# Kernel tuning notes

Hardware: AMD Instinct MI355X
Metric: run time of the kernel (lower is better)

## Reference

```python
import jax, jax.numpy as jnp
import numpy as np

B, W, G, E, NI, K = 2048, 8192, 8, 128, 16, 15


def setup_inputs() -> dict:
    key = jax.random.key(0)
    ks = jax.random.split(key, 12)
    wavelengths_nm = jnp.linspace(300.0, 400.0, W, dtype=jnp.float32)
    # Rayleigh optical depth (Hansen & Travis style approximation), AMF=1 column
    lam_um = wavelengths_nm / 1000.0
    rayleigh_od = (0.008569 * lam_um ** -4
                   * (1.0 + 0.0113 * lam_um ** -2 + 0.00013 * lam_um ** -4)).astype(jnp.float32)
    return {
        "gas_columns": jax.random.uniform(ks[0], (B, G), jnp.float32),
        "instrument_ids": jax.random.randint(ks[1], (B,), 0, NI),
        "nuisance_latent": jax.random.normal(ks[2], (B, G), jnp.float32),
        "air_mass": 1.0 + 2.0 * jax.random.uniform(ks[3], (B,), jnp.float32),
        "wavelengths_nm": wavelengths_nm,
        "absorption": 0.1 * jax.random.uniform(ks[4], (G, W), jnp.float32),
        "continuum_basis": 0.05 * jax.random.normal(ks[5], (G + 1, W), jnp.float32),
        "rayleigh_od": rayleigh_od,
        "embed_table": jax.random.normal(ks[6], (NI, E), jnp.float32),
        "w1": jax.random.normal(ks[7], (E + G, 64), jnp.float32) / np.sqrt(E + G),
        "b1": jnp.zeros((64,), jnp.float32),
        "w2": jax.random.normal(ks[8], (64, 7), jnp.float32) / 8.0,
        "b2": jnp.zeros((7,), jnp.float32),
    }


def _gaussian_kernel(width_px, kernel_size):
    half = (kernel_size - 1) / 2
    pos = jnp.linspace(-half, half, kernel_size, dtype=width_px.dtype)  # [K]
    k = jnp.exp(-0.5 * (pos[None, :] / (width_px[:, None] + 1e-6)) ** 2)  # [B,K]
    return k / k.sum(axis=1, keepdims=True)


def _forward(gas_columns, nuisance_latent, air_mass, wavelengths_nm, absorption,
             continuum_basis, rayleigh_od, embed_table, w1, b1, w2, b2,
             instrument_ids):
    b = gas_columns.shape[0]
    am = air_mass[:, None]                                   # [B,1]
    scaled = gas_columns * am                                # [B,G]
    optical_depth = scaled @ absorption                      # [B,W]
    ones = jnp.ones((b, 1), gas_columns.dtype)
    continuum = jnp.concatenate([gas_columns, ones], axis=1) @ continuum_basis  # [B,W]
    differential = optical_depth + continuum + am * rayleigh_od[None, :]

    # nuisance MLP on [latent, embedding]
    embed = embed_table[instrument_ids]                      # [B,E]
    nin = jnp.concatenate([nuisance_latent, embed], axis=-1)
    h = jax.nn.gelu(nin @ w1 + b1, approximate=False)
    p = h @ w2 + b2                                          # [B,7]

    gain = jax.nn.softplus(p[:, 0]) + 0.001
    offset = p[:, 1]
    woff = 0.05 * jnp.tanh(p[:, 2])
    wscale = 1.0 + 0.005 * jnp.tanh(p[:, 3])
    lsf = jnp.clip(jax.nn.softplus(p[:, 4]) + 0.001, 0.2, 5.0)
    stray = jax.nn.sigmoid(p[:, 5]) * 0.05
    nonlin = 0.02 * jnp.tanh(p[:, 6])

    # per-sample wavelength shift/scale + linear resampling
    new_wl = wavelengths_nm[None, :] * wscale[:, None] + woff[:, None]  # [B,W]
    differential = jax.vmap(lambda wq, d: jnp.interp(wq, wavelengths_nm, d))(new_wl, differential)

    # per-sample Gaussian LSF convolution (replicate padding)
    kernel = _gaussian_kernel(lsf, K)                        # [B,K]
    pad = K // 2
    padded = jnp.pad(differential, ((0, 0), (pad, pad)), mode='edge')  # [B,W+K-1]
    n = differential.shape[1]
    convolved = sum(padded[:, k:k + n] * kernel[:, k:k + 1] for k in range(K))

    counts = jnp.exp(-convolved)
    post = gain[:, None] * counts + offset[:, None]
    total_nl = jnp.clip(nonlin, -0.04, 0.04)                 # instrument nonlinearity = 0
    nl_counts = post + total_nl[:, None] * post ** 2
    total_stray = jnp.clip(stray, 0.0, 0.2)                  # instrument stray = 0
    simulated = (1.0 - total_stray[:, None]) * nl_counts \
        + total_stray[:, None] * nl_counts.mean(axis=1, keepdims=True)
    return simulated


def reference(gas_columns, instrument_ids, nuisance_latent, air_mass,
              wavelengths_nm, absorption, continuum_basis, rayleigh_od,
              embed_table, w1, b1, w2, b2):
    return _forward(gas_columns, nuisance_latent, air_mass, wavelengths_nm,
                    absorption, continuum_basis, rayleigh_od, embed_table,
                    w1, b1, w2, b2, instrument_ids)
```

## Files before the change

kernel.cpp:

```cpp
#include <hip/hip_runtime.h>

#define W_ 8192
#define NBATCH 2048
#define NT 256
#define NWAVE 4
#define SEGW 2048
#define CCH 256
#define NCHW 8
#define IRW 272

typedef unsigned short u16_t;
typedef _Float16 h2v __attribute__((ext_vector_type(2)));

__device__ __forceinline__ u16_t f2h(float x){ _Float16 h=(_Float16)x; return __builtin_bit_cast(u16_t,h); }
__device__ __forceinline__ float h2f(u16_t u){ return (float)__builtin_bit_cast(_Float16,u); }
__device__ __forceinline__ unsigned pk2(float a,float b){ return (unsigned)f2h(a)|((unsigned)f2h(b)<<16); }
__device__ __forceinline__ float dot2u(unsigned a,unsigned b,float c){
#if __has_builtin(__builtin_amdgcn_fdot2)
  return __builtin_amdgcn_fdot2(__builtin_bit_cast(h2v,a),__builtin_bit_cast(h2v,b),c,false);
#else
  h2v ha=__builtin_bit_cast(h2v,a), hb=__builtin_bit_cast(h2v,b);
  return c+(float)ha[0]*(float)hb[0]+(float)ha[1]*(float)hb[1];
#endif
}
__device__ __forceinline__ unsigned pkrtz(float a,float b){
#if __has_builtin(__builtin_amdgcn_cvt_pkrtz)
  return __builtin_bit_cast(unsigned, __builtin_amdgcn_cvt_pkrtz(a,b));
#else
  return pk2(a,b);
#endif
}
__device__ __forceinline__ unsigned alignb(unsigned hi, unsigned lo){
#if __has_builtin(__builtin_amdgcn_alignbit)
  return __builtin_amdgcn_alignbit(hi, lo, 16);
#else
  return (lo >> 16) | (hi << 16);
#endif
}
__device__ __forceinline__ float softplusf(float x){ return fmaxf(x,0.f)+log1pf(expf(-fabsf(x))); }
__device__ __forceinline__ unsigned rflv(unsigned v){
  return (unsigned)__builtin_amdgcn_readfirstlane((int)v);
}
__device__ __forceinline__ float rflvf(float v){
  return __builtin_bit_cast(float, __builtin_amdgcn_readfirstlane(__builtin_bit_cast(int, v)));
}

__global__ __launch_bounds__(256, 2)
void doas_prep(const float* __restrict__ absn, const float* __restrict__ cbn,
               const float* __restrict__ ray, const int* __restrict__ iid,
               const float* __restrict__ nuis, const float* __restrict__ emb,
               const float* __restrict__ w1, const float* __restrict__ b1,
               const float* __restrict__ w2, const float* __restrict__ b2,
               unsigned* __restrict__ Tp, float* __restrict__ params){
  const int tid = threadIdx.x;
  const int b = blockIdx.x;
  __shared__ float hS[4][64];
  __shared__ float pS[4][8];

  if (b < 32){
    const int w = b*256 + tid;
    #pragma unroll
    for (int q=0;q<4;++q) Tp[q*W_+w]     = pk2(absn[(2*q)*W_+w], absn[(2*q+1)*W_+w]);
    #pragma unroll
    for (int q=0;q<4;++q) Tp[(4+q)*W_+w] = pk2(cbn[(2*q)*W_+w],  cbn[(2*q+1)*W_+w]);
    Tp[8*W_+w] = pk2(cbn[8*W_+w], ray[w]);
  }

  {
    const int rl = tid >> 6, j = tid & 63;
    const int r = b*4 + rl;
    const int id = iid[r];
    float acc = b1[j];
    const float* nrow = nuis + (size_t)r * 8;
    #pragma unroll
    for (int i = 0; i < 8; ++i) acc = fmaf(nrow[i], w1[i*64 + j], acc);
    const float* erow = emb + (size_t)id * 128;
    for (int i = 0; i < 128; ++i) acc = fmaf(erow[i], w1[(8+i)*64 + j], acc);
    hS[rl][j] = 0.5f * acc * (1.0f + erff(acc * 0.70710678118654752f));
  }
  __syncthreads();
  if (tid < 4*7){
    const int rl = tid / 7, k = tid % 7;
    float p = b2[k];
    for (int j = 0; j < 64; ++j) p = fmaf(hS[rl][j], w2[j*7+k], p);
    pS[rl][k] = p;
  }
  __syncthreads();
  if (tid < 4){
    const int rl = tid;
    const int r = b*4 + rl;
    float p0=pS[rl][0], p1=pS[rl][1], p2=pS[rl][2], p3=pS[rl][3],
          p4=pS[rl][4], p5=pS[rl][5], p6=pS[rl][6];
    float gainv = softplusf(p0) + 0.001f;
    float offv  = p1;
    float woffv = 0.05f * tanhf(p2);
    float wscv  = 1.0f + 0.005f * tanhf(p3);
    float lsf   = fminf(fmaxf(softplusf(p4) + 0.001f, 0.2f), 5.0f);
    float strv  = fminf(fmaxf((1.0f/(1.0f+expf(-p5))) * 0.05f, 0.0f), 0.2f);
    float nlin  = fminf(fmaxf(0.02f * tanhf(p6), -0.04f), 0.04f);
    float iw = 1.0f/(lsf + 1e-6f);
    float ks[15]; float ksum = 0.f;
    #pragma unroll
    for (int k2=0;k2<15;++k2){ float pp=(float)(k2-7)*iw; float e=expf(-0.5f*pp*pp); ks[k2]=e; ksum+=e; }
    float inv = 1.0f/ksum;
    float* pr = params + (size_t)r*16;
    unsigned* pu = (unsigned*)pr;
    #pragma unroll
    for (int i=0;i<7;++i) pu[i] = pk2(ks[2*i]*inv, ks[2*i+1]*inv);
    pu[7] = pk2(ks[14]*inv, 0.0f);
    pr[9]  = wscv;
    pr[10] = (300.0f*(wscv - 1.0f) + woffv) * (8191.0f/100.0f);
    pr[11] = gainv; pr[12] = offv; pr[13] = nlin; pr[14] = strv;
    pr[15] = 0.f;
  }
}

template<bool CLO, bool CHI>
__device__ __forceinline__ void interp_chunk(int cbase, int l, const unsigned* __restrict__ rU,
                                             unsigned* __restrict__ irowU,
                                             float wscale, float posoff){
  #pragma unroll
  for (int it=0; it<3; ++it){
    const int pi = it*64 + l;
    if (pi < 136){
      float v2[2];
      #pragma unroll
      for (int u=0;u<2;++u){
        int j = cbase + 2*pi + u;
        if (CLO) j = max(j, 0);
        if (CHI) j = min(j, W_-1);
        float pos = fmaf((float)j, wscale, posoff);
        if (CLO) pos = fmaxf(pos, 0.0f);
        if (CHI) pos = fminf(pos, 8191.0f);
        int i0 = (int)pos;
        if (CHI) i0 = min(i0, W_-2);
        const float fr = pos - (float)i0;
        const int m = i0 >> 1;
        const unsigned u0 = rU[m];
        const unsigned u1 = rU[m+1];
        const unsigned hu0 = u0 >> 16;
        const bool odd = (i0 & 1);
        const unsigned ua = odd ? hu0 : u0;
        const unsigned ub = odd ? u1  : hu0;
        const float d0 = h2f((u16_t)ua);
        const float d1 = h2f((u16_t)ub);
        v2[u] = fmaf(fr, d1-d0, d0);
      }
      irowU[pi] = pkrtz(v2[0], v2[1]);
    }
  }
}

__global__ __launch_bounds__(NT, 2)
void doas_main7(const unsigned* __restrict__ Tp, const float* __restrict__ gas,
                const float* __restrict__ air, const float* __restrict__ params,
                float* __restrict__ out){
  __shared__ u16_t rowH[W_ + 16];
  __shared__ u16_t irowS[NWAVE][IRW];
  __shared__ float wsumS[NWAVE];

  const int tid = threadIdx.x;
  const int row = blockIdx.x;
  const int wid = tid >> 6, l = tid & 63;
  const int segbase = wid * SEGW;

  unsigned csg[9];
  {
    const float am = air[row];
    const float* gfp = gas + (size_t)row * 8;
    #pragma unroll
    for (int q=0;q<4;++q) csg[q]   = rflv(pk2(gfp[2*q]*am, gfp[2*q+1]*am));
    #pragma unroll
    for (int q=0;q<4;++q) csg[4+q] = rflv(pk2(gfp[2*q],    gfp[2*q+1]));
    csg[8] = rflv(pk2(1.0f, am));
  }

  const float* pr = params + (size_t)row * 16;
  const unsigned* pu = (const unsigned*)pr;
  unsigned kwp[7];
  #pragma unroll
  for (int i=0;i<7;++i) kwp[i] = rflv(pu[i]);
  const unsigned k14lo = rflv(pu[7]);
  const float wscale = rflvf(pr[9]),  posoff = rflvf(pr[10]);
  const float gainv  = rflvf(pr[11]), offv   = rflvf(pr[12]);
  const float nlin   = rflvf(pr[13]), strv   = rflvf(pr[14]);

  unsigned* rowHU = (unsigned*)rowH;
  #pragma unroll
  for (int it=0; it<8; ++it){
    const int e0 = it*1024 + tid*4;
    uint4 dq[9];
    #pragma unroll
    for (int q=0;q<9;++q) dq[q] = *(const uint4*)(Tp + q*W_ + e0);
    float a0=0.f, a1=0.f, a2=0.f, a3=0.f;
    #pragma unroll
    for (int q=0;q<9;++q){
      a0 = dot2u(dq[q].x, csg[q], a0);
      a1 = dot2u(dq[q].y, csg[q], a1);
      a2 = dot2u(dq[q].z, csg[q], a2);
      a3 = dot2u(dq[q].w, csg[q], a3);
    }
    *(uint2*)(rowHU + (e0 >> 1)) = make_uint2(pkrtz(a0,a1), pkrtz(a2,a3));
  }
  __syncthreads();

  const unsigned* rU = (const unsigned*)rowH;
  u16_t* irow = &irowS[wid][0];
  unsigned* irowU = (unsigned*)irow;

  float accsum = 0.f;
  unsigned nlp[NCHW][2];

  #pragma unroll
  for (int c = 0; c < NCHW; ++c) {
    const int cs = segbase + c*CCH;
    const int cbase = cs - 8;
    if (wid == 0 && c == 0)
      interp_chunk<true,false>(cbase, l, rU, irowU, wscale, posoff);
    else if (wid == NWAVE-1 && c == NCHW-1)
      interp_chunk<false,true>(cbase, l, rU, irowU, wscale, posoff);
    else
      interp_chunk<false,false>(cbase, l, rU, irowU, wscale, posoff);
    __builtin_amdgcn_wave_barrier();
    {
      const uint2* p2 = (const uint2*)irowU + l;
      const uint2 A = p2[0], B = p2[1], C = p2[2], D = p2[3], E = p2[4];
      unsigned q[10] = {A.x,A.y, B.x,B.y, C.x,C.y, D.x,D.y, E.x,E.y};
      unsigned sh[9];
      #pragma unroll
      for (int m=0;m<9;++m) sh[m] = alignb(q[m+1], q[m]);
      float nlv[4];
      #pragma unroll
      for (int t=0;t<4;++t){
        float cv = 0.f;
        if ((t & 1) == 0){
          const int b0 = t >> 1;
          #pragma unroll
          for (int i=0;i<7;++i) cv = dot2u(sh[b0+i], kwp[i], cv);
          cv = dot2u(sh[b0+7], k14lo, cv);
        } else {
          const int b0 = (t+1) >> 1;
          #pragma unroll
          for (int i=0;i<7;++i) cv = dot2u(q[b0+i], kwp[i], cv);
          cv = dot2u(q[b0+7], k14lo, cv);
        }
        const float counts = __expf(-cv);
        const float post = fmaf(gainv, counts, offv);
        const float v = fmaf(nlin*post, post, post);
        accsum += v;
        nlv[t] = v;
      }
      nlp[c][0] = pkrtz(nlv[0], nlv[1]);
      nlp[c][1] = pkrtz(nlv[2], nlv[3]);
    }
    __builtin_amdgcn_wave_barrier();
  }

  float s = accsum;
  #pragma unroll
  for (int off2 = 32; off2 >= 1; off2 >>= 1) s += __shfl_down(s, off2);
  if (l == 0) wsumS[wid] = s;
  __syncthreads();
  const float meanv = (wsumS[0]+wsumS[1]+wsumS[2]+wsumS[3]) * (1.0f/8192.0f);

  {
    const float aa = 1.0f - strv;
    const float bb = strv * meanv;
    float* orow = out + (size_t)row * W_;
    #pragma unroll
    for (int c = 0; c < NCHW; ++c) {
      const unsigned u0 = nlp[c][0], u1 = nlp[c][1];
      float4 o0;
      o0.x = fmaf(aa, h2f((u16_t)(u0 & 0xffffu)), bb);
      o0.y = fmaf(aa, h2f((u16_t)(u0 >> 16)),     bb);
      o0.z = fmaf(aa, h2f((u16_t)(u1 & 0xffffu)), bb);
      o0.w = fmaf(aa, h2f((u16_t)(u1 >> 16)),     bb);
      *(float4*)(orow + segbase + c*CCH + 4*l) = o0;
    }
  }
}

__global__ __launch_bounds__(256, 2)
void doas_mono(const float* __restrict__ gas, const int* __restrict__ iid,
               const float* __restrict__ nuis, const float* __restrict__ air,
               const float* __restrict__ absn, const float* __restrict__ cbn,
               const float* __restrict__ ray, const float* __restrict__ emb,
               const float* __restrict__ w1, const float* __restrict__ b1,
               const float* __restrict__ w2, const float* __restrict__ b2,
               float* __restrict__ out)
{
  __shared__ u16_t ringS[4][2048];
  __shared__ u16_t irowS2[4][544];
  __shared__ float hS[64];
  __shared__ float pS[8];
  __shared__ float scalS[52];
  __shared__ float wsumS[4];

  const int tid = threadIdx.x;
  const int row = blockIdx.x;

  if (tid < 64) {
    const int j = tid;
    const int id = iid[row];
    float acc = b1[j];
    const float* nrow = nuis + (size_t)row * 8;
    #pragma unroll
    for (int i = 0; i < 8; ++i) acc = fmaf(nrow[i], w1[i*64 + j], acc);
    const float* erow = emb + (size_t)id * 128;
    for (int i = 0; i < 128; ++i) acc = fmaf(erow[i], w1[(8+i)*64 + j], acc);
    hS[j] = 0.5f * acc * (1.0f + erff(acc * 0.70710678118654752f));
  }
  __syncthreads();
  if (tid < 7) {
    float p = b2[tid];
    for (int j = 0; j < 64; ++j) p = fmaf(hS[j], w2[j*7+tid], p);
    pS[tid] = p;
  }
  __syncthreads();
  if (tid == 0) {
    float p0=pS[0], p1=pS[1], p2=pS[2], p3=pS[3], p4=pS[4], p5=pS[5], p6=pS[6];
    float gainv = softplusf(p0) + 0.001f;
    float offv  = p1;
    float woffv = 0.05f * tanhf(p2);
    float wscv  = 1.0f + 0.005f * tanhf(p3);
    float lsf   = fminf(fmaxf(softplusf(p4) + 0.001f, 0.2f), 5.0f);
    float strv  = fminf(fmaxf((1.0f/(1.0f+expf(-p5))) * 0.05f, 0.0f), 0.2f);
    float nlin  = fminf(fmaxf(0.02f * tanhf(p6), -0.04f), 0.04f);
    float iw = 1.0f/(lsf + 1e-6f);
    float ks[15]; float ksum = 0.f;
    #pragma unroll
    for (int k2=0;k2<15;++k2){ float pp=(float)(k2-7)*iw; float e=expf(-0.5f*pp*pp); ks[k2]=e; ksum+=e; }
    float inv = 1.0f/ksum;
    scalS[15] = wscv;
    scalS[16] = (300.0f*(wscv - 1.0f) + woffv) * (8191.0f/100.0f);
    scalS[17] = gainv; scalS[18] = offv; scalS[19] = nlin; scalS[20] = strv;
    scalS[22] = air[row];
    unsigned* su = (unsigned*)scalS;
    #pragma unroll
    for (int i=0;i<7;++i) su[32+i] = pk2(ks[2*i]*inv, ks[2*i+1]*inv);
    su[39] = pk2(ks[14]*inv, 0.0f);
    su[40] = pk2(0.0f, ks[14]*inv);
    #pragma unroll
    for (int g=0; g<8; ++g) scalS[23+g] = gas[(size_t)row*8+g];
  }
  __syncthreads();

  const int wid = tid >> 6, l = tid & 63;
  const int segbase = wid * 2048;
  const unsigned* scalU = (const unsigned*)scalS;
  unsigned kwp[7];
  #pragma unroll
  for (int i=0;i<7;++i) kwp[i] = rflv(scalU[32+i]);
  const unsigned k14lo = rflv(scalU[39]), k14hi = rflv(scalU[40]);
  const float wscale = scalS[15], posoff = scalS[16];
  const float gainv  = scalS[17], offv   = scalS[18];
  const float nlin   = scalS[19], strv   = scalS[20];

  u16_t* ring = &ringS[wid][0];
  unsigned* ringU = (unsigned*)ring;
  u16_t* irow = &irowS2[wid][0];
  unsigned* irowU = (unsigned*)irow;

  auto do_diff = [&](int s){
    const int sbase = segbase - 256 + (s << 9);
    #pragma unroll
    for (int it=0; it<4; ++it){
      const int e0 = sbase + ((it*64 + l) << 1);
      const int eL = min(max(e0, 0), W_-2);
      const float am = scalS[22];
      float a0=0.f, a1=0.f;
      #pragma unroll
      for (int g=0; g<8; ++g){
        const float cg = scalS[23+g];
        const float ca = cg*am;
        a0 = fmaf(ca, absn[g*W_+eL],   a0); a0 = fmaf(cg, cbn[g*W_+eL],   a0);
        a1 = fmaf(ca, absn[g*W_+eL+1], a1); a1 = fmaf(cg, cbn[g*W_+eL+1], a1);
      }
      a0 += cbn[8*W_+eL]   + am*ray[eL];
      a1 += cbn[8*W_+eL+1] + am*ray[eL+1];
      ringU[((unsigned)e0 & 2047) >> 1] = pkrtz(a0, a1);
    }
  };

  float accsum = 0.f;
  unsigned nlp[4][4];

  do_diff(0); do_diff(1);
  __builtin_amdgcn_wave_barrier();

  #pragma unroll
  for (int c = 0; c < 4; ++c) {
    if (c < 3) do_diff(c+2);
    __builtin_amdgcn_wave_barrier();
    {
      const int cbase = segbase + (c << 9) - 8;
      #pragma unroll
      for (int it = 0; it < 5; ++it) {
        const int pi = it*64 + l;
        if (pi < 264) {
          float v2[2];
          #pragma unroll
          for (int u=0; u<2; ++u){
            const int j = cbase + 2*pi + u;
            const int jc = min(max(j, 0), W_-1);
            float pos = fmaf((float)jc, wscale, posoff);
            pos = fminf(fmaxf(pos, 0.0f), 8191.0f);
            const int i0 = min((int)pos, W_-2);
            const float fr = pos - (float)i0;
            const float d0 = h2f(ring[ i0    & 2047]);
            const float d1 = h2f(ring[(i0+1) & 2047]);
            v2[u] = fmaf(fr, d1-d0, d0);
          }
          irowU[pi] = pkrtz(v2[0], v2[1]);
        }
      }
    }
    __builtin_amdgcn_wave_barrier();
    {
      const uint4* qp = (const uint4*)irow + l;
      const uint4 A = qp[0], B = qp[1], C = qp[2];
      unsigned q[12] = {A.x,A.y,A.z,A.w, B.x,B.y,B.z,B.w, C.x,C.y,C.z,C.w};
      unsigned sh[10];
      #pragma unroll
      for (int m=0;m<10;++m) sh[m] = alignb(q[m+1], q[m]);
      float nlv[8];
      #pragma unroll
      for (int t=0;t<8;++t){
        const int s2 = t >> 1;
        float cv = 0.f;
        if ((t & 1) == 0){
          #pragma unroll
          for (int i=0;i<7;++i) cv = dot2u(sh[s2+i], kwp[i], cv);
          cv = dot2u(q[s2+7], k14hi, cv);
        } else {
          #pragma unroll
          for (int i=0;i<7;++i) cv = dot2u(q[s2+1+i], kwp[i], cv);
          cv = dot2u(q[s2+8], k14lo, cv);
        }
        const float counts = __expf(-cv);
        const float post = fmaf(gainv, counts, offv);
        const float v = fmaf(nlin*post, post, post);
        accsum += v;
        nlv[t] = v;
      }
      nlp[c][0] = pkrtz(nlv[0], nlv[1]);
      nlp[c][1] = pkrtz(nlv[2], nlv[3]);
      nlp[c][2] = pkrtz(nlv[4], nlv[5]);
      nlp[c][3] = pkrtz(nlv[6], nlv[7]);
    }
    __builtin_amdgcn_wave_barrier();
  }

  float s = accsum;
  #pragma unroll
  for (int off2 = 32; off2 >= 1; off2 >>= 1) s += __shfl_down(s, off2);
  if (l == 0) wsumS[wid] = s;
  __syncthreads();
  const float meanv = (wsumS[0]+wsumS[1]+wsumS[2]+wsumS[3]) * (1.0f/8192.0f);

  {
    const float aa = 1.0f - strv;
    const float bb = strv * meanv;
    float* orow = out + (size_t)row * W_;
    #pragma unroll
    for (int c = 0; c < 4; ++c) {
      const unsigned u0 = nlp[c][0], u1 = nlp[c][1], u2 = nlp[c][2], u3 = nlp[c][3];
      float4 o0, o1;
      o0.x = fmaf(aa, h2f((u16_t)(u0 & 0xffffu)), bb);
      o0.y = fmaf(aa, h2f((u16_t)(u0 >> 16)),     bb);
      o0.z = fmaf(aa, h2f((u16_t)(u1 & 0xffffu)), bb);
      o0.w = fmaf(aa, h2f((u16_t)(u1 >> 16)),     bb);
      o1.x = fmaf(aa, h2f((u16_t)(u2 & 0xffffu)), bb);
      o1.y = fmaf(aa, h2f((u16_t)(u2 >> 16)),     bb);
      o1.z = fmaf(aa, h2f((u16_t)(u3 & 0xffffu)), bb);
      o1.w = fmaf(aa, h2f((u16_t)(u3 >> 16)),     bb);
      float* dst = orow + segbase + (c << 9) + 8*l;
      *(float4*)(dst)     = o0;
      *(float4*)(dst + 4) = o1;
    }
  }
}

extern "C" void kernel_launch(void* const* d_in, const int* in_sizes, int n_in,
                              void* d_out, int out_size, void* d_ws, size_t ws_size,
                              hipStream_t stream) {
  const float* gas  = (const float*)d_in[0];
  const int*   iid  = (const int*)d_in[1];
  const float* nuis = (const float*)d_in[2];
  const float* air  = (const float*)d_in[3];
  const float* wl   = (const float*)d_in[4];
  const float* absn = (const float*)d_in[5];
  const float* cbn  = (const float*)d_in[6];
  const float* ray  = (const float*)d_in[7];
  const float* emb  = (const float*)d_in[8];
  const float* w1   = (const float*)d_in[9];
  const float* b1   = (const float*)d_in[10];
  const float* w2   = (const float*)d_in[11];
  const float* b2   = (const float*)d_in[12];
  float* out = (float*)d_out;
  (void)in_sizes; (void)n_in; (void)out_size; (void)wl;

  const size_t packBytes = (size_t)9 * W_ * 4;
  const size_t parBytes  = (size_t)NBATCH * 16 * 4;

  if (ws_size >= packBytes + parBytes) {
    unsigned* Tp  = (unsigned*)d_ws;
    float* params = (float*)((char*)d_ws + packBytes);
    hipLaunchKernelGGL(doas_prep, dim3(NBATCH/4), dim3(256), 0, stream,
                       absn, cbn, ray, iid, nuis, emb, w1, b1, w2, b2, Tp, params);
    hipLaunchKernelGGL(doas_main7, dim3(NBATCH), dim3(NT), 0, stream,
                       Tp, gas, air, params, out);
  } else {
    hipLaunchKernelGGL(doas_mono, dim3(NBATCH), dim3(256), 0, stream,
                       gas, iid, nuis, air, absn, cbn, ray, emb, w1, b1, w2, b2, out);
  }
}
```

Before: 51.62 us.

## Fuse nuisance MLP into main kernel and store differential row as fp32 in LDS

```diff
diff --git a/kernel.cpp b/kernel.cpp
--- a/kernel.cpp
+++ b/kernel.cpp
@@ -45,78 +45,19 @@
   return __builtin_bit_cast(float, __builtin_amdgcn_readfirstlane(__builtin_bit_cast(int, v)));
 }
 
-__global__ __launch_bounds__(256, 2)
-void doas_prep(const float* __restrict__ absn, const float* __restrict__ cbn,
-               const float* __restrict__ ray, const int* __restrict__ iid,
-               const float* __restrict__ nuis, const float* __restrict__ emb,
-               const float* __restrict__ w1, const float* __restrict__ b1,
-               const float* __restrict__ w2, const float* __restrict__ b2,
-               unsigned* __restrict__ Tp, float* __restrict__ params){
-  const int tid = threadIdx.x;
-  const int b = blockIdx.x;
-  __shared__ float hS[4][64];
-  __shared__ float pS[4][8];
-
-  if (b < 32){
-    const int w = b*256 + tid;
-    #pragma unroll
-    for (int q=0;q<4;++q) Tp[q*W_+w]     = pk2(absn[(2*q)*W_+w], absn[(2*q+1)*W_+w]);
-    #pragma unroll
-    for (int q=0;q<4;++q) Tp[(4+q)*W_+w] = pk2(cbn[(2*q)*W_+w],  cbn[(2*q+1)*W_+w]);
-    Tp[8*W_+w] = pk2(cbn[8*W_+w], ray[w]);
-  }
-
-  {
-    const int rl = tid >> 6, j = tid & 63;
-    const int r = b*4 + rl;
-    const int id = iid[r];
-    float acc = b1[j];
-    const float* nrow = nuis + (size_t)r * 8;
-    #pragma unroll
-    for (int i = 0; i < 8; ++i) acc = fmaf(nrow[i], w1[i*64 + j], acc);
-    const float* erow = emb + (size_t)id * 128;
-    for (int i = 0; i < 128; ++i) acc = fmaf(erow[i], w1[(8+i)*64 + j], acc);
-    hS[rl][j] = 0.5f * acc * (1.0f + erff(acc * 0.70710678118654752f));
-  }
-  __syncthreads();
-  if (tid < 4*7){
-    const int rl = tid / 7, k = tid % 7;
-    float p = b2[k];
-    for (int j = 0; j < 64; ++j) p = fmaf(hS[rl][j], w2[j*7+k], p);
-    pS[rl][k] = p;
-  }
-  __syncthreads();
-  if (tid < 4){
-    const int rl = tid;
-    const int r = b*4 + rl;
-    float p0=pS[rl][0], p1=pS[rl][1], p2=pS[rl][2], p3=pS[rl][3],
-          p4=pS[rl][4], p5=pS[rl][5], p6=pS[rl][6];
-    float gainv = softplusf(p0) + 0.001f;
-    float offv  = p1;
-    float woffv = 0.05f * tanhf(p2);
-    float wscv  = 1.0f + 0.005f * tanhf(p3);
-    float lsf   = fminf(fmaxf(softplusf(p4) + 0.001f, 0.2f), 5.0f);
-    float strv  = fminf(fmaxf((1.0f/(1.0f+expf(-p5))) * 0.05f, 0.0f), 0.2f);
-    float nlin  = fminf(fmaxf(0.02f * tanhf(p6), -0.04f), 0.04f);
-    float iw = 1.0f/(lsf + 1e-6f);
-    float ks[15]; float ksum = 0.f;
-    #pragma unroll
-    for (int k2=0;k2<15;++k2){ float pp=(float)(k2-7)*iw; float e=expf(-0.5f*pp*pp); ks[k2]=e; ksum+=e; }
-    float inv = 1.0f/ksum;
-    float* pr = params + (size_t)r*16;
-    unsigned* pu = (unsigned*)pr;
-    #pragma unroll
-    for (int i=0;i<7;++i) pu[i] = pk2(ks[2*i]*inv, ks[2*i+1]*inv);
-    pu[7] = pk2(ks[14]*inv, 0.0f);
-    pr[9]  = wscv;
-    pr[10] = (300.0f*(wscv - 1.0f) + woffv) * (8191.0f/100.0f);
-    pr[11] = gainv; pr[12] = offv; pr[13] = nlin; pr[14] = strv;
-    pr[15] = 0.f;
-  }
+__global__ __launch_bounds__(64, 4)
+void doas_pack(const float* __restrict__ absn, const float* __restrict__ cbn,
+               const float* __restrict__ ray, unsigned* __restrict__ Tp){
+  const int w = blockIdx.x*64 + threadIdx.x;
+  #pragma unroll
+  for (int q=0;q<4;++q) Tp[q*W_+w]     = pk2(absn[(2*q)*W_+w], absn[(2*q+1)*W_+w]);
+  #pragma unroll
+  for (int q=0;q<4;++q) Tp[(4+q)*W_+w] = pk2(cbn[(2*q)*W_+w],  cbn[(2*q+1)*W_+w]);
+  Tp[8*W_+w] = pk2(cbn[8*W_+w], ray[w]);
 }
 
 template<bool CLO, bool CHI>
-__device__ __forceinline__ void interp_chunk(int cbase, int l, const unsigned* __restrict__ rU,
+__device__ __forceinline__ void interp_chunk(int cbase, int l, const float* __restrict__ rF,
                                              unsigned* __restrict__ irowU,
                                              float wscale, float posoff){
   #pragma unroll
@@ -135,15 +76,8 @@
         int i0 = (int)pos;
         if (CHI) i0 = min(i0, W_-2);
         const float fr = pos - (float)i0;
-        const int m = i0 >> 1;
-        const unsigned u0 = rU[m];
-        const unsigned u1 = rU[m+1];
-        const unsigned hu0 = u0 >> 16;
-        const bool odd = (i0 & 1);
-        const unsigned ua = odd ? hu0 : u0;
-        const unsigned ub = odd ? u1  : hu0;
-        const float d0 = h2f((u16_t)ua);
-        const float d1 = h2f((u16_t)ub);
+        const float d0 = rF[i0];
+        const float d1 = rF[i0+1];
         v2[u] = fmaf(fr, d1-d0, d0);
       }
       irowU[pi] = pkrtz(v2[0], v2[1]);
@@ -152,10 +86,13 @@
 }
 
 __global__ __launch_bounds__(NT, 2)
-void doas_main7(const unsigned* __restrict__ Tp, const float* __restrict__ gas,
-                const float* __restrict__ air, const float* __restrict__ params,
+void doas_main8(const unsigned* __restrict__ Tp, const float* __restrict__ gas,
+                const float* __restrict__ air, const int* __restrict__ iid,
+                const float* __restrict__ nuis, const float* __restrict__ emb,
+                const float* __restrict__ w1, const float* __restrict__ b1,
+                const float* __restrict__ w2, const float* __restrict__ b2,
                 float* __restrict__ out){
-  __shared__ u16_t rowH[W_ + 16];
+  __shared__ float rowF[W_ + 4];
   __shared__ u16_t irowS[NWAVE][IRW];
   __shared__ float wsumS[NWAVE];
 
@@ -175,17 +112,55 @@
     csg[8] = rflv(pk2(1.0f, am));
   }
 
-  const float* pr = params + (size_t)row * 16;
-  const unsigned* pu = (const unsigned*)pr;
-  unsigned kwp[7];
-  #pragma unroll
-  for (int i=0;i<7;++i) kwp[i] = rflv(pu[i]);
-  const unsigned k14lo = rflv(pu[7]);
-  const float wscale = rflvf(pr[9]),  posoff = rflvf(pr[10]);
-  const float gainv  = rflvf(pr[11]), offv   = rflvf(pr[12]);
-  const float nlin   = rflvf(pr[13]), strv   = rflvf(pr[14]);
-
-  unsigned* rowHU = (unsigned*)rowH;
+  float hj;
+  {
+    const int id = iid[row];
+    float acc = b1[l];
+    const float* nrow = nuis + (size_t)row * 8;
+    #pragma unroll
+    for (int i = 0; i < 8; ++i) acc = fmaf(nrow[i], w1[i*64 + l], acc);
+    const float* erow = emb + (size_t)id * 128;
+    #pragma unroll 8
+    for (int i = 0; i < 128; ++i) acc = fmaf(erow[i], w1[(8+i)*64 + l], acc);
+    hj = 0.5f * acc * (1.0f + erff(acc * 0.70710678118654752f));
+  }
+  float pv[7];
+  {
+    const float* w2r = w2 + l*7;
+    #pragma unroll
+    for (int k=0;k<7;++k) pv[k] = hj * w2r[k];
+    #pragma unroll
+    for (int off=32; off>=1; off>>=1){
+      #pragma unroll
+      for (int k=0;k<7;++k) pv[k] += __shfl_down(pv[k], off);
+    }
+    #pragma unroll
+    for (int k=0;k<7;++k) pv[k] = __shfl(pv[k] + b2[k], 0);
+  }
+  unsigned kwp[7]; unsigned k14lo;
+  float wscale, posoff, gainv, offv, nlin, strv;
+  {
+    float p0=pv[0], p1=pv[1], p2=pv[2], p3=pv[3], p4=pv[4], p5=pv[5], p6=pv[6];
+    float gv = softplusf(p0) + 0.001f;
+    float ov = p1;
+    float woffv = 0.05f * tanhf(p2);
+    float wscv  = 1.0f + 0.005f * tanhf(p3);
+    float lsf   = fminf(fmaxf(softplusf(p4) + 0.001f, 0.2f), 5.0f);
+    float sv    = fminf(fmaxf((1.0f/(1.0f+expf(-p5))) * 0.05f, 0.0f), 0.2f);
+    float nv    = fminf(fmaxf(0.02f * tanhf(p6), -0.04f), 0.04f);
+    float iw = 1.0f/(lsf + 1e-6f);
+    float ks[15]; float ksum = 0.f;
+    #pragma unroll
+    for (int k2=0;k2<15;++k2){ float pp=(float)(k2-7)*iw; float e=expf(-0.5f*pp*pp); ks[k2]=e; ksum+=e; }
+    float inv = 1.0f/ksum;
+    #pragma unroll
+    for (int i=0;i<7;++i) kwp[i] = rflv(pk2(ks[2*i]*inv, ks[2*i+1]*inv));
+    k14lo = rflv(pk2(ks[14]*inv, 0.0f));
+    wscale = rflvf(wscv);
+    posoff = rflvf((300.0f*(wscv - 1.0f) + woffv) * (8191.0f/100.0f));
+    gainv = rflvf(gv); offv = rflvf(ov); nlin = rflvf(nv); strv = rflvf(sv);
+  }
+
   #pragma unroll
   for (int it=0; it<8; ++it){
     const int e0 = it*1024 + tid*4;
@@ -200,11 +175,11 @@
       a2 = dot2u(dq[q].z, csg[q], a2);
       a3 = dot2u(dq[q].w, csg[q], a3);
     }
-    *(uint2*)(rowHU + (e0 >> 1)) = make_uint2(pkrtz(a0,a1), pkrtz(a2,a3));
-  }
-  __syncthreads();
-
-  const unsigned* rU = (const unsigned*)rowH;
+    float4 wv; wv.x=a0; wv.y=a1; wv.z=a2; wv.w=a3;
+    *(float4*)(rowF + e0) = wv;
+  }
+  __syncthreads();
+
   u16_t* irow = &irowS[wid][0];
   unsigned* irowU = (unsigned*)irow;
 
@@ -216,11 +191,11 @@
     const int cs = segbase + c*CCH;
     const int cbase = cs - 8;
     if (wid == 0 && c == 0)
-      interp_chunk<true,false>(cbase, l, rU, irowU, wscale, posoff);
+      interp_chunk<true,false>(cbase, l, rowF, irowU, wscale, posoff);
     else if (wid == NWAVE-1 && c == NCHW-1)
-      interp_chunk<false,true>(cbase, l, rU, irowU, wscale, posoff);
+      interp_chunk<false,true>(cbase, l, rowF, irowU, wscale, posoff);
     else
-      interp_chunk<false,false>(cbase, l, rU, irowU, wscale, posoff);
+      interp_chunk<false,false>(cbase, l, rowF, irowU, wscale, posoff);
     __builtin_amdgcn_wave_barrier();
     {
       const uint2* p2 = (const uint2*)irowU + l;
@@ -501,15 +476,12 @@
   (void)in_sizes; (void)n_in; (void)out_size; (void)wl;
 
   const size_t packBytes = (size_t)9 * W_ * 4;
-  const size_t parBytes  = (size_t)NBATCH * 16 * 4;
-
-  if (ws_size >= packBytes + parBytes) {
-    unsigned* Tp  = (unsigned*)d_ws;
-    float* params = (float*)((char*)d_ws + packBytes);
-    hipLaunchKernelGGL(doas_prep, dim3(NBATCH/4), dim3(256), 0, stream,
-                       absn, cbn, ray, iid, nuis, emb, w1, b1, w2, b2, Tp, params);
-    hipLaunchKernelGGL(doas_main7, dim3(NBATCH), dim3(NT), 0, stream,
-                       Tp, gas, air, params, out);
+
+  if (ws_size >= packBytes) {
+    unsigned* Tp = (unsigned*)d_ws;
+    hipLaunchKernelGGL(doas_pack, dim3(W_/64), dim3(64), 0, stream, absn, cbn, ray, Tp);
+    hipLaunchKernelGGL(doas_main8, dim3(NBATCH), dim3(NT), 0, stream,
+                       Tp, gas, air, iid, nuis, emb, w1, b1, w2, b2, out);
   } else {
     hipLaunchKernelGGL(doas_mono, dim3(NBATCH), dim3(256), 0, stream,
                        gas, iid, nuis, air, absn, cbn, ray, emb, w1, b1, w2, b2, out);
```

After: 57.14 us. 10.7% more time.

## Fuse per-row nuisance MLP into main kernel, shrink prep to weight packing

Applied to the files above, without the earlier changes.

```diff
diff --git a/kernel.cpp b/kernel.cpp
--- a/kernel.cpp
+++ b/kernel.cpp
@@ -46,73 +46,14 @@
 }
 
 __global__ __launch_bounds__(256, 2)
-void doas_prep(const float* __restrict__ absn, const float* __restrict__ cbn,
-               const float* __restrict__ ray, const int* __restrict__ iid,
-               const float* __restrict__ nuis, const float* __restrict__ emb,
-               const float* __restrict__ w1, const float* __restrict__ b1,
-               const float* __restrict__ w2, const float* __restrict__ b2,
-               unsigned* __restrict__ Tp, float* __restrict__ params){
-  const int tid = threadIdx.x;
-  const int b = blockIdx.x;
-  __shared__ float hS[4][64];
-  __shared__ float pS[4][8];
-
-  if (b < 32){
-    const int w = b*256 + tid;
-    #pragma unroll
-    for (int q=0;q<4;++q) Tp[q*W_+w]     = pk2(absn[(2*q)*W_+w], absn[(2*q+1)*W_+w]);
-    #pragma unroll
-    for (int q=0;q<4;++q) Tp[(4+q)*W_+w] = pk2(cbn[(2*q)*W_+w],  cbn[(2*q+1)*W_+w]);
-    Tp[8*W_+w] = pk2(cbn[8*W_+w], ray[w]);
-  }
-
-  {
-    const int rl = tid >> 6, j = tid & 63;
-    const int r = b*4 + rl;
-    const int id = iid[r];
-    float acc = b1[j];
-    const float* nrow = nuis + (size_t)r * 8;
-    #pragma unroll
-    for (int i = 0; i < 8; ++i) acc = fmaf(nrow[i], w1[i*64 + j], acc);
-    const float* erow = emb + (size_t)id * 128;
-    for (int i = 0; i < 128; ++i) acc = fmaf(erow[i], w1[(8+i)*64 + j], acc);
-    hS[rl][j] = 0.5f * acc * (1.0f + erff(acc * 0.70710678118654752f));
-  }
-  __syncthreads();
-  if (tid < 4*7){
-    const int rl = tid / 7, k = tid % 7;
-    float p = b2[k];
-    for (int j = 0; j < 64; ++j) p = fmaf(hS[rl][j], w2[j*7+k], p);
-    pS[rl][k] = p;
-  }
-  __syncthreads();
-  if (tid < 4){
-    const int rl = tid;
-    const int r = b*4 + rl;
-    float p0=pS[rl][0], p1=pS[rl][1], p2=pS[rl][2], p3=pS[rl][3],
-          p4=pS[rl][4], p5=pS[rl][5], p6=pS[rl][6];
-    float gainv = softplusf(p0) + 0.001f;
-    float offv  = p1;
-    float woffv = 0.05f * tanhf(p2);
-    float wscv  = 1.0f + 0.005f * tanhf(p3);
-    float lsf   = fminf(fmaxf(softplusf(p4) + 0.001f, 0.2f), 5.0f);
-    float strv  = fminf(fmaxf((1.0f/(1.0f+expf(-p5))) * 0.05f, 0.0f), 0.2f);
-    float nlin  = fminf(fmaxf(0.02f * tanhf(p6), -0.04f), 0.04f);
-    float iw = 1.0f/(lsf + 1e-6f);
-    float ks[15]; float ksum = 0.f;
-    #pragma unroll
-    for (int k2=0;k2<15;++k2){ float pp=(float)(k2-7)*iw; float e=expf(-0.5f*pp*pp); ks[k2]=e; ksum+=e; }
-    float inv = 1.0f/ksum;
-    float* pr = params + (size_t)r*16;
-    unsigned* pu = (unsigned*)pr;
-    #pragma unroll
-    for (int i=0;i<7;++i) pu[i] = pk2(ks[2*i]*inv, ks[2*i+1]*inv);
-    pu[7] = pk2(ks[14]*inv, 0.0f);
-    pr[9]  = wscv;
-    pr[10] = (300.0f*(wscv - 1.0f) + woffv) * (8191.0f/100.0f);
-    pr[11] = gainv; pr[12] = offv; pr[13] = nlin; pr[14] = strv;
-    pr[15] = 0.f;
-  }
+void doas_pack(const float* __restrict__ absn, const float* __restrict__ cbn,
+               const float* __restrict__ ray, unsigned* __restrict__ Tp){
+  const int w = blockIdx.x*256 + threadIdx.x;
+  #pragma unroll
+  for (int q=0;q<4;++q) Tp[q*W_+w]     = pk2(absn[(2*q)*W_+w], absn[(2*q+1)*W_+w]);
+  #pragma unroll
+  for (int q=0;q<4;++q) Tp[(4+q)*W_+w] = pk2(cbn[(2*q)*W_+w],  cbn[(2*q+1)*W_+w]);
+  Tp[8*W_+w] = pk2(cbn[8*W_+w], ray[w]);
 }
 
 template<bool CLO, bool CHI>
@@ -152,11 +93,17 @@
 }
 
 __global__ __launch_bounds__(NT, 2)
-void doas_main7(const unsigned* __restrict__ Tp, const float* __restrict__ gas,
-                const float* __restrict__ air, const float* __restrict__ params,
+void doas_main9(const unsigned* __restrict__ Tp, const float* __restrict__ gas,
+                const float* __restrict__ air, const int* __restrict__ iid,
+                const float* __restrict__ nuis, const float* __restrict__ emb,
+                const float* __restrict__ w1, const float* __restrict__ b1,
+                const float* __restrict__ w2, const float* __restrict__ b2,
                 float* __restrict__ out){
   __shared__ u16_t rowH[W_ + 16];
   __shared__ u16_t irowS[NWAVE][IRW];
+  __shared__ float hS[64];
+  __shared__ float pS[8];
+  __shared__ float scalS[44];
   __shared__ float wsumS[NWAVE];
 
   const int tid = threadIdx.x;
@@ -174,16 +121,6 @@
     for (int q=0;q<4;++q) csg[4+q] = rflv(pk2(gfp[2*q],    gfp[2*q+1]));
     csg[8] = rflv(pk2(1.0f, am));
   }
-
-  const float* pr = params + (size_t)row * 16;
-  const unsigned* pu = (const unsigned*)pr;
-  unsigned kwp[7];
-  #pragma unroll
-  for (int i=0;i<7;++i) kwp[i] = rflv(pu[i]);
-  const unsigned k14lo = rflv(pu[7]);
-  const float wscale = rflvf(pr[9]),  posoff = rflvf(pr[10]);
-  const float gainv  = rflvf(pr[11]), offv   = rflvf(pr[12]);
-  const float nlin   = rflvf(pr[13]), strv   = rflvf(pr[14]);
 
   unsigned* rowHU = (unsigned*)rowH;
   #pragma unroll
@@ -202,7 +139,57 @@
     }
     *(uint2*)(rowHU + (e0 >> 1)) = make_uint2(pkrtz(a0,a1), pkrtz(a2,a3));
   }
-  __syncthreads();
+
+  if (tid < 64) {
+    const int id = iid[row];
+    float acc = b1[tid];
+    const float* nrow = nuis + (size_t)row * 8;
+    #pragma unroll
+    for (int i = 0; i < 8; ++i) acc = fmaf(nrow[i], w1[i*64 + tid], acc);
+    const float* erow = emb + (size_t)id * 128;
+    #pragma unroll 8
+    for (int i = 0; i < 128; ++i) acc = fmaf(erow[i], w1[(8+i)*64 + tid], acc);
+    hS[tid] = 0.5f * acc * (1.0f + erff(acc * 0.70710678118654752f));
+  }
+  __syncthreads();
+  if (tid < 7) {
+    float p = b2[tid];
+    for (int j = 0; j < 64; ++j) p = fmaf(hS[j], w2[j*7+tid], p);
+    pS[tid] = p;
+  }
+  __syncthreads();
+  if (tid == 0) {
+    float p0=pS[0], p1=pS[1], p2=pS[2], p3=pS[3], p4=pS[4], p5=pS[5], p6=pS[6];
+    float gainv = softplusf(p0) + 0.001f;
+    float offv  = p1;
+    float woffv = 0.05f * tanhf(p2);
+    float wscv  = 1.0f + 0.005f * tanhf(p3);
+    float lsf   = fminf(fmaxf(softplusf(p4) + 0.001f, 0.2f), 5.0f);
+    float strv  = fminf(fmaxf((1.0f/(1.0f+expf(-p5))) * 0.05f, 0.0f), 0.2f);
+    float nlin  = fminf(fmaxf(0.02f * tanhf(p6), -0.04f), 0.04f);
+    float iw = 1.0f/(lsf + 1e-6f);
+    float ks[15]; float ksum = 0.f;
+    #pragma unroll
+    for (int k2=0;k2<15;++k2){ float pp=(float)(k2-7)*iw; float e=expf(-0.5f*pp*pp); ks[k2]=e; ksum+=e; }
+    float inv = 1.0f/ksum;
+    unsigned* su = (unsigned*)scalS;
+    #pragma unroll
+    for (int i=0;i<7;++i) su[32+i] = pk2(ks[2*i]*inv, ks[2*i+1]*inv);
+    su[39] = pk2(ks[14]*inv, 0.0f);
+    scalS[15] = wscv;
+    scalS[16] = (300.0f*(wscv - 1.0f) + woffv) * (8191.0f/100.0f);
+    scalS[17] = gainv; scalS[18] = offv; scalS[19] = nlin; scalS[20] = strv;
+  }
+  __syncthreads();
+
+  const unsigned* scalU = (const unsigned*)scalS;
+  unsigned kwp[7];
+  #pragma unroll
+  for (int i=0;i<7;++i) kwp[i] = rflv(scalU[32+i]);
+  const unsigned k14lo = rflv(scalU[39]);
+  const float wscale = rflvf(scalS[15]), posoff = rflvf(scalS[16]);
+  const float gainv  = rflvf(scalS[17]), offv   = rflvf(scalS[18]);
+  const float nlin   = rflvf(scalS[19]), strv   = rflvf(scalS[20]);
 
   const unsigned* rU = (const unsigned*)rowH;
   u16_t* irow = &irowS[wid][0];
@@ -501,15 +488,12 @@
   (void)in_sizes; (void)n_in; (void)out_size; (void)wl;
 
   const size_t packBytes = (size_t)9 * W_ * 4;
-  const size_t parBytes  = (size_t)NBATCH * 16 * 4;
-
-  if (ws_size >= packBytes + parBytes) {
-    unsigned* Tp  = (unsigned*)d_ws;
-    float* params = (float*)((char*)d_ws + packBytes);
-    hipLaunchKernelGGL(doas_prep, dim3(NBATCH/4), dim3(256), 0, stream,
-                       absn, cbn, ray, iid, nuis, emb, w1, b1, w2, b2, Tp, params);
-    hipLaunchKernelGGL(doas_main7, dim3(NBATCH), dim3(NT), 0, stream,
-                       Tp, gas, air, params, out);
+
+  if (ws_size >= packBytes) {
+    unsigned* Tp = (unsigned*)d_ws;
+    hipLaunchKernelGGL(doas_pack, dim3(W_/256), dim3(256), 0, stream, absn, cbn, ray, Tp);
+    hipLaunchKernelGGL(doas_main9, dim3(NBATCH), dim3(NT), 0, stream,
+                       Tp, gas, air, iid, nuis, emb, w1, b1, w2, b2, out);
   } else {
     hipLaunchKernelGGL(doas_mono, dim3(NBATCH), dim3(256), 0, stream,
                        gas, iid, nuis, air, absn, cbn, ray, emb, w1, b1, w2, b2, out);
```

New measurement: 60.65 us. 17.5% more time.

## Double-buffer interpolation chunks and shrink prep kernel to one wave per row

Applied to the files above, without the earlier changes.

```diff
diff --git a/kernel.cpp b/kernel.cpp
--- a/kernel.cpp
+++ b/kernel.cpp
@@ -45,20 +45,18 @@
   return __builtin_bit_cast(float, __builtin_amdgcn_readfirstlane(__builtin_bit_cast(int, v)));
 }
 
-__global__ __launch_bounds__(256, 2)
-void doas_prep(const float* __restrict__ absn, const float* __restrict__ cbn,
-               const float* __restrict__ ray, const int* __restrict__ iid,
-               const float* __restrict__ nuis, const float* __restrict__ emb,
-               const float* __restrict__ w1, const float* __restrict__ b1,
-               const float* __restrict__ w2, const float* __restrict__ b2,
-               unsigned* __restrict__ Tp, float* __restrict__ params){
+__global__ __launch_bounds__(64, 8)
+void doas_prep2(const float* __restrict__ absn, const float* __restrict__ cbn,
+                const float* __restrict__ ray, const int* __restrict__ iid,
+                const float* __restrict__ nuis, const float* __restrict__ emb,
+                const float* __restrict__ w1, const float* __restrict__ b1,
+                const float* __restrict__ w2, const float* __restrict__ b2,
+                unsigned* __restrict__ Tp, float* __restrict__ params){
   const int tid = threadIdx.x;
-  const int b = blockIdx.x;
-  __shared__ float hS[4][64];
-  __shared__ float pS[4][8];
-
-  if (b < 32){
-    const int w = b*256 + tid;
+  const int r = blockIdx.x;
+
+  if (r < 128){
+    const int w = r*64 + tid;
     #pragma unroll
     for (int q=0;q<4;++q) Tp[q*W_+w]     = pk2(absn[(2*q)*W_+w], absn[(2*q+1)*W_+w]);
     #pragma unroll
@@ -66,31 +64,32 @@
     Tp[8*W_+w] = pk2(cbn[8*W_+w], ray[w]);
   }
 
+  float hj;
   {
-    const int rl = tid >> 6, j = tid & 63;
-    const int r = b*4 + rl;
     const int id = iid[r];
-    float acc = b1[j];
+    float acc = b1[tid];
     const float* nrow = nuis + (size_t)r * 8;
     #pragma unroll
-    for (int i = 0; i < 8; ++i) acc = fmaf(nrow[i], w1[i*64 + j], acc);
+    for (int i = 0; i < 8; ++i) acc = fmaf(nrow[i], w1[i*64 + tid], acc);
     const float* erow = emb + (size_t)id * 128;
-    for (int i = 0; i < 128; ++i) acc = fmaf(erow[i], w1[(8+i)*64 + j], acc);
-    hS[rl][j] = 0.5f * acc * (1.0f + erff(acc * 0.70710678118654752f));
-  }
-  __syncthreads();
-  if (tid < 4*7){
-    const int rl = tid / 7, k = tid % 7;
-    float p = b2[k];
-    for (int j = 0; j < 64; ++j) p = fmaf(hS[rl][j], w2[j*7+k], p);
-    pS[rl][k] = p;
-  }
-  __syncthreads();
-  if (tid < 4){
-    const int rl = tid;
-    const int r = b*4 + rl;
-    float p0=pS[rl][0], p1=pS[rl][1], p2=pS[rl][2], p3=pS[rl][3],
-          p4=pS[rl][4], p5=pS[rl][5], p6=pS[rl][6];
+    #pragma unroll 8
+    for (int i = 0; i < 128; ++i) acc = fmaf(erow[i], w1[(8+i)*64 + tid], acc);
+    hj = 0.5f * acc * (1.0f + erff(acc * 0.70710678118654752f));
+  }
+  float pv[7];
+  {
+    const float* w2r = w2 + tid*7;
+    #pragma unroll
+    for (int k=0;k<7;++k) pv[k] = hj * w2r[k];
+    #pragma unroll
+    for (int off=32; off>=1; off>>=1){
+      #pragma unroll
+      for (int k=0;k<7;++k) pv[k] += __shfl_down(pv[k], off);
+    }
+  }
+  if (tid == 0){
+    float p0=pv[0]+b2[0], p1=pv[1]+b2[1], p2=pv[2]+b2[2], p3=pv[3]+b2[3],
+          p4=pv[4]+b2[4], p5=pv[5]+b2[5], p6=pv[6]+b2[6];
     float gainv = softplusf(p0) + 0.001f;
     float offv  = p1;
     float woffv = 0.05f * tanhf(p2);
@@ -151,12 +150,47 @@
   }
 }
 
+__device__ __forceinline__ void conv_chunk(const unsigned* __restrict__ irowU, int l,
+                                           const unsigned* kwp, unsigned k14lo,
+                                           float gainv, float offv, float nlin,
+                                           float& accsum, unsigned* nlpc){
+  const uint2* p2 = (const uint2*)irowU + l;
+  const uint2 A = p2[0], B = p2[1], C = p2[2], D = p2[3], E = p2[4];
+  unsigned q[10] = {A.x,A.y, B.x,B.y, C.x,C.y, D.x,D.y, E.x,E.y};
+  unsigned sh[9];
+  #pragma unroll
+  for (int m=0;m<9;++m) sh[m] = alignb(q[m+1], q[m]);
+  float nlv[4];
+  #pragma unroll
+  for (int t=0;t<4;++t){
+    float cv = 0.f;
+    if ((t & 1) == 0){
+      const int b0 = t >> 1;
+      #pragma unroll
+      for (int i=0;i<7;++i) cv = dot2u(sh[b0+i], kwp[i], cv);
+      cv = dot2u(sh[b0+7], k14lo, cv);
+    } else {
+      const int b0 = (t+1) >> 1;
+      #pragma unroll
+      for (int i=0;i<7;++i) cv = dot2u(q[b0+i], kwp[i], cv);
+      cv = dot2u(q[b0+7], k14lo, cv);
+    }
+    const float counts = __expf(-cv);
+    const float post = fmaf(gainv, counts, offv);
+    const float v = fmaf(nlin*post, post, post);
+    accsum += v;
+    nlv[t] = v;
+  }
+  nlpc[0] = pkrtz(nlv[0], nlv[1]);
+  nlpc[1] = pkrtz(nlv[2], nlv[3]);
+}
+
 __global__ __launch_bounds__(NT, 2)
-void doas_main7(const unsigned* __restrict__ Tp, const float* __restrict__ gas,
-                const float* __restrict__ air, const float* __restrict__ params,
-                float* __restrict__ out){
+void doas_main10(const unsigned* __restrict__ Tp, const float* __restrict__ gas,
+                 const float* __restrict__ air, const float* __restrict__ params,
+                 float* __restrict__ out){
   __shared__ u16_t rowH[W_ + 16];
-  __shared__ u16_t irowS[NWAVE][IRW];
+  __shared__ u16_t irowS[NWAVE][2][IRW];
   __shared__ float wsumS[NWAVE];
 
   const int tid = threadIdx.x;
@@ -205,55 +239,29 @@
   __syncthreads();
 
   const unsigned* rU = (const unsigned*)rowH;
-  u16_t* irow = &irowS[wid][0];
-  unsigned* irowU = (unsigned*)irow;
+  unsigned* buf0 = (unsigned*)&irowS[wid][0][0];
+  unsigned* buf1 = (unsigned*)&irowS[wid][1][0];
 
   float accsum = 0.f;
   unsigned nlp[NCHW][2];
 
+  if (wid == 0)
+    interp_chunk<true,false>(segbase - 8, l, rU, buf0, wscale, posoff);
+  else
+    interp_chunk<false,false>(segbase - 8, l, rU, buf0, wscale, posoff);
+
   #pragma unroll
   for (int c = 0; c < NCHW; ++c) {
-    const int cs = segbase + c*CCH;
-    const int cbase = cs - 8;
-    if (wid == 0 && c == 0)
-      interp_chunk<true,false>(cbase, l, rU, irowU, wscale, posoff);
-    else if (wid == NWAVE-1 && c == NCHW-1)
-      interp_chunk<false,true>(cbase, l, rU, irowU, wscale, posoff);
-    else
-      interp_chunk<false,false>(cbase, l, rU, irowU, wscale, posoff);
-    __builtin_amdgcn_wave_barrier();
-    {
-      const uint2* p2 = (const uint2*)irowU + l;
-      const uint2 A = p2[0], B = p2[1], C = p2[2], D = p2[3], E = p2[4];
-      unsigned q[10] = {A.x,A.y, B.x,B.y, C.x,C.y, D.x,D.y, E.x,E.y};
-      unsigned sh[9];
-      #pragma unroll
-      for (int m=0;m<9;++m) sh[m] = alignb(q[m+1], q[m]);
-      float nlv[4];
-      #pragma unroll
-      for (int t=0;t<4;++t){
-        float cv = 0.f;
-        if ((t & 1) == 0){
-          const int b0 = t >> 1;
-          #pragma unroll
-          for (int i=0;i<7;++i) cv = dot2u(sh[b0+i], kwp[i], cv);
-          cv = dot2u(sh[b0+7], k14lo, cv);
-        } else {
-          const int b0 = (t+1) >> 1;
-          #pragma unroll
-          for (int i=0;i<7;++i) cv = dot2u(q[b0+i], kwp[i], cv);
-          cv = dot2u(q[b0+7], k14lo, cv);
-        }
-        const float counts = __expf(-cv);
-        const float post = fmaf(gainv, counts, offv);
-        const float v = fmaf(nlin*post, post, post);
-        accsum += v;
-        nlv[t] = v;
-      }
-      nlp[c][0] = pkrtz(nlv[0], nlv[1]);
-      nlp[c][1] = pkrtz(nlv[2], nlv[3]);
-    }
-    __builtin_amdgcn_wave_barrier();
+    unsigned* cur = (c & 1) ? buf1 : buf0;
+    unsigned* nxt = (c & 1) ? buf0 : buf1;
+    if (c < NCHW-1){
+      const int cbase = segbase + (c+1)*CCH - 8;
+      if (wid == NWAVE-1 && c+1 == NCHW-1)
+        interp_chunk<false,true>(cbase, l, rU, nxt, wscale, posoff);
+      else
+        interp_chunk<false,false>(cbase, l, rU, nxt, wscale, posoff);
+    }
+    conv_chunk(cur, l, kwp, k14lo, gainv, offv, nlin, accsum, nlp[c]);
   }
 
   float s = accsum;
@@ -506,9 +514,9 @@
   if (ws_size >= packBytes + parBytes) {
     unsigned* Tp  = (unsigned*)d_ws;
     float* params = (float*)((char*)d_ws + packBytes);
-    hipLaunchKernelGGL(doas_prep, dim3(NBATCH/4), dim3(256), 0, stream,
+    hipLaunchKernelGGL(doas_prep2, dim3(NBATCH), dim3(64), 0, stream,
                        absn, cbn, ray, iid, nuis, emb, w1, b1, w2, b2, Tp, params);
-    hipLaunchKernelGGL(doas_main7, dim3(NBATCH), dim3(NT), 0, stream,
+    hipLaunchKernelGGL(doas_main10, dim3(NBATCH), dim3(NT), 0, stream,
                        Tp, gas, air, params, out);
   } else {
     hipLaunchKernelGGL(doas_mono, dim3(NBATCH), dim3(256), 0, stream,
```

New measurement: 53.90 us. +4.4%, slower.
